# Kernel optimization log

Measured on AMD Instinct MI355X. Metric: run time of the kernel, lower is better.

The kernel has to match this reference:

```python
import jax, jax.numpy as jnp
import numpy as np
from jax import lax

BS, L, NB = 16, 50, 64          # batch, seq_length, num_blk_pervisit
D = 256                          # d_model
BLK_D = 768                      # frozen block-embedding dim
N_BLK = 65536                    # block vocab size
MEM_SIZE = 64                    # mem_size == mem_update_size (required for stackable memory)
MEM_UPDATE = 64
EPS = 1e-5


def _blk_trans(x, w1, b1, w2, b2, g, b):
    # Linear(768->2D) + ReLU + Linear(2D->D) + LayerNorm(D); dropout omitted (eval mode)
    h = jax.nn.relu(x @ w1 + b1)
    y = h @ w2 + b2
    mu = jnp.mean(y, axis=-1, keepdims=True)
    var = jnp.mean((y - mu) ** 2, axis=-1, keepdims=True)
    return g * (y - mu) * lax.rsqrt(var + EPS) + b


def setup_inputs() -> dict:
    key = jax.random.key(0)
    ks = jax.random.split(key, 16)
    s = 0.02
    f32 = jnp.float32
    return {
        "v_all": jax.random.normal(ks[0], (BS, L, D), f32),
        "transformed_v_all": jax.random.normal(ks[1], (BS, L, D), f32),
        "blk_emb_w": jax.random.normal(ks[2], (N_BLK, BLK_D), f32) * s,
        "bt_w1": jax.random.normal(ks[3], (BLK_D, 2 * D), f32) * s,
        "bt_b1": jnp.zeros((2 * D,), f32),
        "bt_w2": jax.random.normal(ks[4], (2 * D, D), f32) * s,
        "bt_b2": jnp.zeros((D,), f32),
        "bt_g": jnp.ones((D,), f32),
        "bt_b": jnp.zeros((D,), f32),
        "wq": jax.random.normal(ks[5], (D, D), f32) * s,
        "wk": jax.random.normal(ks[6], (D, D), f32) * s,
        "am_w1": jax.random.normal(ks[7], (2 * D, D), f32) * s,
        "am_b1": jnp.zeros((D,), f32),
        "am_w2": jax.random.normal(ks[8], (D, 1), f32) * s,
        "out_w": jax.random.normal(ks[9], (2 * D, 2), f32) * s,
        "out_b": jnp.zeros((2,), f32),
        "input_txt": jax.random.randint(ks[10], (BS, L, NB), 0, N_BLK, dtype=jnp.int32),
        "masks_txt": jax.random.randint(ks[11], (BS, L, NB), 0, 2, dtype=jnp.int32),
        "lengths": jax.random.randint(ks[12], (BS,), 2, L + 1, dtype=jnp.int32),
    }


def reference(v_all, transformed_v_all, blk_emb_w, bt_w1, bt_b1, bt_w2, bt_b2,
              bt_g, bt_b, wq, wk, am_w1, am_b1, am_w2, out_w, out_b,
              input_txt, masks_txt, lengths):
    bt = (bt_w1, bt_b1, bt_w2, bt_b2, bt_g, bt_b)

    # --- per-visit block selection (att_mlp + topk gather) ---
    v_text = _blk_trans(blk_emb_w[input_txt], *bt)                 # [BS,L,NB,D]
    tv = jnp.broadcast_to(transformed_v_all[:, :, None, :], v_text.shape)
    att_in = jnp.concatenate([tv, v_text], axis=-1)                # [BS,L,NB,2D]
    score = (jnp.tanh(att_in @ am_w1 + am_b1) @ am_w2)[..., 0]     # [BS,L,NB]
    score = jax.nn.softmax(score, axis=-1)
    score = jnp.where(masks_txt == 0, 0.0, score)
    idx = lax.top_k(score, MEM_UPDATE)[1]                          # [BS,L,MU]
    sel_ids = jnp.take_along_axis(input_txt, idx, axis=2)          # [BS,L,MU]
    sel_mask = jnp.take_along_axis(masks_txt, idx, axis=2)

    # --- sequential memory update recurrence ---
    query = transformed_v_all + v_all                              # [BS,L,D]
    scale = jnp.sqrt(jnp.float32(D))

    def step(carry, xs):
        ids, mk = carry                                            # [BS, M]
        nids, nmk, q = xs                                          # [BS,MU], [BS,MU], [BS,D]
        mem_in = jnp.concatenate([ids, nids], axis=1)              # [BS, 2M]
        mask_in = jnp.concatenate([mk, nmk], axis=1)
        x = _blk_trans(blk_emb_w[mem_in], *bt)                     # [BS,2M,D]
        e = jnp.einsum("bd,bmd->bm", q @ wq, x @ wk) / scale
        att = jnp.where(mask_in == 0, 0.0, jax.nn.softmax(e, axis=-1))
        tki = lax.top_k(att, MEM_SIZE)[1]                          # [BS, M]
        oi = jnp.take_along_axis(mem_in, tki, axis=1)
        om = jnp.take_along_axis(mask_in, tki, axis=1)
        return (oi, om), oi

    xs = (jnp.swapaxes(sel_ids[:, 1:], 0, 1),
          jnp.swapaxes(sel_mask[:, 1:], 0, 1),
          jnp.swapaxes(query[:, 1:], 0, 1))
    _, ys = lax.scan(step, (sel_ids[:, 0], sel_mask[:, 0]), xs)    # [L-1,BS,M]
    mem_stack = jnp.swapaxes(ys, 0, 1)                             # [BS,L-1,M] == memory[1:]
    memory_final = jnp.take_along_axis(
        mem_stack, (lengths - 2)[:, None, None], axis=1)[:, 0]      # [BS,M]

    # --- pooling + output head ---
    vmask = jnp.arange(L)[None, :] < lengths[:, None]              # length-masked max pool
    v_final = jnp.max(jnp.where(vmask[:, :, None], transformed_v_all, -jnp.inf), axis=1)
    mem_vec_final = jnp.max(_blk_trans(blk_emb_w[memory_final], *bt), axis=1)
    output = jnp.concatenate([v_final, mem_vec_final], axis=1) @ out_w + out_b
    return (output, memory_final)
```

## Files before the change

### kernel.cpp

```cpp
#include <hip/hip_runtime.h>
#include <math.h>

constexpr int kBS   = 16;
constexpr int kL    = 50;
constexpr int kNB   = 64;
constexpr int kD    = 256;
constexpr int kNBLK = 65536;
constexpr int kMaxUsed = 51200;

#define NEG_HUGE (-3.402823466e38f)

typedef _Float16 h8 __attribute__((ext_vector_type(8)));
typedef float f32x4 __attribute__((ext_vector_type(4)));

__device__ __forceinline__ unsigned f2sort(float f) {
    unsigned u = __float_as_uint(f);
    return (u & 0x80000000u) ? ~u : (u | 0x80000000u);
}

__device__ __forceinline__ void bitonic_u64(unsigned long long* s, int i, int n) {
    for (int k = 2; k <= n; k <<= 1) {
        for (int j = k >> 1; j > 0; j >>= 1) {
            __syncthreads();
            int ixj = i ^ j;
            if (ixj > i) {
                unsigned long long x = s[i], y = s[ixj];
                bool sw = ((i & k) == 0) ? (x > y) : (x < y);
                if (sw) { s[i] = y; s[ixj] = x; }
            }
        }
    }
    __syncthreads();
}

__device__ __forceinline__ void split8(const float4& a, const float4& b, float s,
                                       h8& hh, h8& ll) {
    float v0 = a.x * s, v1 = a.y * s, v2 = a.z * s, v3 = a.w * s;
    float v4 = b.x * s, v5 = b.y * s, v6 = b.z * s, v7 = b.w * s;
    hh[0] = (_Float16)v0; ll[0] = (_Float16)(v0 - (float)hh[0]);
    hh[1] = (_Float16)v1; ll[1] = (_Float16)(v1 - (float)hh[1]);
    hh[2] = (_Float16)v2; ll[2] = (_Float16)(v2 - (float)hh[2]);
    hh[3] = (_Float16)v3; ll[3] = (_Float16)(v3 - (float)hh[3]);
    hh[4] = (_Float16)v4; ll[4] = (_Float16)(v4 - (float)hh[4]);
    hh[5] = (_Float16)v5; ll[5] = (_Float16)(v5 - (float)hh[5]);
    hh[6] = (_Float16)v6; ll[6] = (_Float16)(v6 - (float)hh[6]);
    hh[7] = (_Float16)v7; ll[7] = (_Float16)(v7 - (float)hh[7]);
}

__global__ void k_clear(int* __restrict__ flags) {
    flags[blockIdx.x * 256 + threadIdx.x] = 0;
}
__global__ void k_mark(const int* __restrict__ ids, int* __restrict__ flags, int n) {
    int i = blockIdx.x * 256 + threadIdx.x;
    if (i < n) flags[ids[i]] = 1;
}
__global__ void k_scan_a(const int* __restrict__ flags, int* __restrict__ slots,
                         int* __restrict__ bsum) {
    int i = blockIdx.x * 256 + threadIdx.x;
    __shared__ int s[256];
    int v = flags[i];
    s[threadIdx.x] = v; __syncthreads();
    for (int o = 1; o < 256; o <<= 1) {
        int t2 = (threadIdx.x >= o) ? s[threadIdx.x - o] : 0;
        __syncthreads();
        s[threadIdx.x] += t2;
        __syncthreads();
    }
    slots[i] = s[threadIdx.x] - v;
    if (threadIdx.x == 255) bsum[blockIdx.x] = s[255];
}
__global__ void k_scan_b(int* __restrict__ bsum, int* __restrict__ mcount) {
    __shared__ int s[256];
    int v = bsum[threadIdx.x];
    s[threadIdx.x] = v; __syncthreads();
    for (int o = 1; o < 256; o <<= 1) {
        int t2 = (threadIdx.x >= o) ? s[threadIdx.x - o] : 0;
        __syncthreads();
        s[threadIdx.x] += t2;
        __syncthreads();
    }
    bsum[threadIdx.x] = s[threadIdx.x] - v;
    if (threadIdx.x == 255) *mcount = s[255];
}
__global__ void k_scan_c(const int* __restrict__ flags, int* __restrict__ slots,
                         const int* __restrict__ bsum, int* __restrict__ ulist) {
    int i = blockIdx.x * 256 + threadIdx.x;
    int slot = slots[i] + bsum[blockIdx.x];
    slots[i] = slot;
    if (flags[i]) ulist[slot] = i;
}

__global__ void k_split_bT(const float* __restrict__ B, int ldb, int K,
                           _Float16* __restrict__ Ph, _Float16* __restrict__ Pl,
                           int row_off, int ldp, float scale)
{
    int n = blockIdx.x;
    for (int k = threadIdx.x; k < K; k += 256) {
        float v = B[(long long)k * ldb + n] * scale;
        _Float16 h = (_Float16)v;
        _Float16 l = (_Float16)(v - (float)h);
        Ph[(long long)(row_off + n) * ldp + k] = h;
        Pl[(long long)(row_off + n) * ldp + k] = l;
    }
}

__global__ __launch_bounds__(256) void gemm_mfma3(
    const float* __restrict__ A, int lda,
    const int* __restrict__ gather, const float* __restrict__ A2,
    const _Float16* __restrict__ Bh, const _Float16* __restrict__ Bl,
    float* __restrict__ C, int ldc,
    int Mstatic, const int* __restrict__ mcount,
    int K, const float* __restrict__ bias, int relu,
    float ascale, float inv_scale)
{
    int mlim = Mstatic;
    if (mcount) mlim = *mcount;
    const int bm = blockIdx.x * 128;
    if (bm >= mlim) return;
    const int bn = blockIdx.y * 128;

    __shared__ h8 AsH[512];
    __shared__ h8 AsL[512];
    __shared__ h8 BsH[512];
    __shared__ h8 BsL[512];

    const int t = threadIdx.x;
    const int lane = t & 63;
    const int wid  = t >> 6;
    const int aRt = (wid >> 1) * 4;
    const int bRt = (wid & 1) * 4;
    const int wr = (wid >> 1) * 64, wc = (wid & 1) * 64;

    const float* aptr[2];
    const float* aptr2[2];
    int awslot[2];
    #pragma unroll
    for (int i = 0; i < 2; ++i) {
        int c = t + i * 256;
        int r = c >> 2, ks = c & 3;
        awslot[i] = (r >> 4) * 64 + (r & 15) + 16 * ks;
        int grow = bm + r;
        long long g = 0;
        if (grow < mlim) g = gather ? (long long)gather[grow] : (long long)grow;
        aptr[i]  = A + g * lda + ks * 8;
        aptr2[i] = A2 ? (A2 + g * lda + ks * 8) : nullptr;
    }
    const _Float16* bptr[4];
    int bwslot[4], bpl[4];
    #pragma unroll
    for (int i = 0; i < 4; ++i) {
        int c = t + i * 256;
        int pl = c >> 9, cc = c & 511;
        int r = cc >> 2, ks = cc & 3;
        bwslot[i] = (r >> 4) * 64 + (r & 15) + 16 * ks;
        bpl[i] = pl;
        bptr[i] = (pl ? Bl : Bh) + (long long)(bn + r) * K + ks * 8;
    }

    f32x4 acc[4][4];
    #pragma unroll
    for (int m = 0; m < 4; ++m)
        #pragma unroll
        for (int n = 0; n < 4; ++n)
            acc[m][n] = (f32x4){0.f, 0.f, 0.f, 0.f};

    float4 pa[2][2], pa2[2][2];
    h8 pb[4];
    #pragma unroll
    for (int i = 0; i < 2; ++i) {
        pa[i][0] = *(const float4*)(aptr[i]);
        pa[i][1] = *(const float4*)(aptr[i] + 4);
        if (A2) {
            pa2[i][0] = *(const float4*)(aptr2[i]);
            pa2[i][1] = *(const float4*)(aptr2[i] + 4);
        }
    }
    #pragma unroll
    for (int i = 0; i < 4; ++i) pb[i] = *(const h8*)(bptr[i]);

    const int nt = K / 32;
    for (int tI = 0; tI < nt; ++tI) {
        __syncthreads();
        #pragma unroll
        for (int i = 0; i < 2; ++i) {
            float4 x = pa[i][0], y = pa[i][1];
            if (A2) {
                x.x += pa2[i][0].x; x.y += pa2[i][0].y;
                x.z += pa2[i][0].z; x.w += pa2[i][0].w;
                y.x += pa2[i][1].x; y.y += pa2[i][1].y;
                y.z += pa2[i][1].z; y.w += pa2[i][1].w;
            }
            h8 hh, ll;
            split8(x, y, ascale, hh, ll);
            AsH[awslot[i]] = hh;
            AsL[awslot[i]] = ll;
        }
        #pragma unroll
        for (int i = 0; i < 4; ++i) {
            (bpl[i] ? BsL : BsH)[bwslot[i]] = pb[i];
        }
        __syncthreads();
        if (tI + 1 < nt) {
            int k0 = (tI + 1) * 32;
            #pragma unroll
            for (int i = 0; i < 2; ++i) {
                pa[i][0] = *(const float4*)(aptr[i] + k0);
                pa[i][1] = *(const float4*)(aptr[i] + k0 + 4);
                if (A2) {
                    pa2[i][0] = *(const float4*)(aptr2[i] + k0);
                    pa2[i][1] = *(const float4*)(aptr2[i] + k0 + 4);
                }
            }
            #pragma unroll
            for (int i = 0; i < 4; ++i) pb[i] = *(const h8*)(bptr[i] + k0);
        }
        h8 ah_[4], al_[4];
        #pragma unroll
        for (int m = 0; m < 4; ++m) {
            ah_[m] = AsH[(aRt + m) * 64 + lane];
            al_[m] = AsL[(aRt + m) * 64 + lane];
        }
        #pragma unroll
        for (int n = 0; n < 4; ++n) {
            h8 bh_ = BsH[(bRt + n) * 64 + lane];
            h8 bl_ = BsL[(bRt + n) * 64 + lane];
            #pragma unroll
            for (int m = 0; m < 4; ++m) {
                acc[m][n] = __builtin_amdgcn_mfma_f32_16x16x32_f16(ah_[m], bh_, acc[m][n], 0, 0, 0);
                acc[m][n] = __builtin_amdgcn_mfma_f32_16x16x32_f16(ah_[m], bl_, acc[m][n], 0, 0, 0);
                acc[m][n] = __builtin_amdgcn_mfma_f32_16x16x32_f16(al_[m], bh_, acc[m][n], 0, 0, 0);
            }
        }
    }

    const int fr  = lane & 15;
    const int cr0 = (lane >> 4) * 4;
    #pragma unroll
    for (int m = 0; m < 4; ++m) {
        #pragma unroll
        for (int r = 0; r < 4; ++r) {
            int row = bm + wr + m * 16 + cr0 + r;
            if (row >= mlim) continue;
            float* crow = C + (long long)row * ldc;
            #pragma unroll
            for (int n = 0; n < 4; ++n) {
                int col = bn + wc + n * 16 + fr;
                float v = acc[m][n][r] * inv_scale;
                if (bias) v += bias[col];
                if (relu) v = fmaxf(v, 0.f);
                crow[col] = v;
            }
        }
    }
}

__global__ __launch_bounds__(256) void ln256_inplace(
    float* __restrict__ Y, const float* __restrict__ g, const float* __restrict__ b,
    int Mstatic, const int* __restrict__ mcount)
{
    int row = blockIdx.x;
    int mlim = mcount ? *mcount : Mstatic;
    if (row >= mlim) return;
    int d = threadIdx.x;
    float v = Y[(long long)row * 256 + d];
    __shared__ float red[256];
    red[d] = v; __syncthreads();
    for (int off = 128; off; off >>= 1) { if (d < off) red[d] += red[d + off]; __syncthreads(); }
    float mu = red[0] * (1.f / 256.f);
    __syncthreads();
    float dv = v - mu;
    red[d] = dv * dv; __syncthreads();
    for (int off = 128; off; off >>= 1) { if (d < off) red[d] += red[d + off]; __syncthreads(); }
    float var = red[0] * (1.f / 256.f);
    float out = g[d] * dv * (1.f / sqrtf(var + 1e-5f)) + b[d];
    Y[(long long)row * 256 + d] = out;
}

__global__ __launch_bounds__(256) void p1score(
    const float* __restrict__ tvp, const float* __restrict__ AK,
    const int* __restrict__ slots, const float* __restrict__ am_w2,
    const int* __restrict__ ids, float* __restrict__ scores)
{
    int bl = blockIdx.x;
    int lane = threadIdx.x & 63;
    int wv   = threadIdx.x >> 6;
    float4 tv = *(const float4*)(tvp + (long long)bl * 256 + lane * 4);
    float4 w2 = *(const float4*)(am_w2 + lane * 4);
    for (int s = wv * 16; s < wv * 16 + 16; ++s) {
        int slot = slots[ids[bl * 64 + s]];
        float4 a = *(const float4*)(AK + (long long)slot * 512 + lane * 4);
        double p = (double)tanhf(tv.x + a.x) * w2.x
                 + (double)tanhf(tv.y + a.y) * w2.y
                 + (double)tanhf(tv.z + a.z) * w2.z
                 + (double)tanhf(tv.w + a.w) * w2.w;
        #pragma unroll
        for (int off = 32; off; off >>= 1) p += __shfl_down(p, off);
        if (lane == 0) scores[bl * 64 + s] = (float)p;
    }
}

__global__ __launch_bounds__(64) void p1sort(
    const float* __restrict__ scores, const int* __restrict__ ids_in,
    const int* __restrict__ mk_in, int* __restrict__ sel_ids, int* __restrict__ sel_mk)
{
    int bl = blockIdx.x;
    int i = threadIdx.x;
    __shared__ unsigned long long s[64];
    float sc = scores[bl * 64 + i];
    int mk = mk_in[bl * 64 + i];
    float key = mk ? sc : NEG_HUGE;
    s[i] = ((unsigned long long)(~f2sort(key)) << 32) | (unsigned)i;
    bitonic_u64(s, i, 64);
    int src = (int)(unsigned)(s[i] & 0xffffffffull);
    sel_ids[bl * 64 + i] = ids_in[bl * 64 + src];
    sel_mk [bl * 64 + i] = mk_in [bl * 64 + src];
}

__global__ __launch_bounds__(256) void etab2(
    const float* __restrict__ qw, const float* __restrict__ AK,
    const int* __restrict__ slots, const int* __restrict__ sel_ids,
    float* __restrict__ E)
{
    const int l = blockIdx.x;
    const int b = blockIdx.y;
    __shared__ float Ks[16][64];
    __shared__ float Qs[16][68];
    __shared__ int rowA[64];
    const int t  = threadIdx.x;
    const int tx = t & 15, ty = t >> 4;
    if (t < 64) rowA[t] = slots[sel_ids[(b * kL + l) * 64 + t]];
    __syncthreads();

    const int rA = t >> 2;
    const int kA = (t & 3) * 4;
    const float* aptr = AK + (long long)rowA[rA] * 512 + 256 + kA;
    const float* qbase = qw + ((long long)b * kL + 1) * 256;
    const bool tsok = rA < 49;

    double acc[4][4];
    #pragma unroll
    for (int i = 0; i < 4; ++i)
        #pragma unroll
        for (int j = 0; j < 4; ++j) acc[i][j] = 0.0;

    for (int k0 = 0; k0 < 256; k0 += 16) {
        float4 av = *(const float4*)(aptr + k0);
        float4 bv = make_float4(0.f, 0.f, 0.f, 0.f);
        if (tsok) bv = *(const float4*)(qbase + (long long)rA * 256 + k0 + kA);
        __syncthreads();
        Ks[kA + 0][rA] = av.x; Ks[kA + 1][rA] = av.y;
        Ks[kA + 2][rA] = av.z; Ks[kA + 3][rA] = av.w;
        Qs[kA + 0][rA] = bv.x; Qs[kA + 1][rA] = bv.y;
        Qs[kA + 2][rA] = bv.z; Qs[kA + 3][rA] = bv.w;
        __syncthreads();
        #pragma unroll
        for (int k = 0; k < 16; ++k) {
            float a[4], q[4];
            *(float4*)&a[0] = *(const float4*)&Ks[k][tx * 4];
            *(float4*)&q[0] = *(const float4*)&Qs[k][ty * 4];
            #pragma unroll
            for (int i = 0; i < 4; ++i)
                #pragma unroll
                for (int j = 0; j < 4; ++j)
                    acc[i][j] += (double)a[i] * (double)q[j];
        }
    }
    #pragma unroll
    for (int j = 0; j < 4; ++j) {
        int ts = ty * 4 + j;
        if (ts >= 49) continue;
        #pragma unroll
        for (int i = 0; i < 4; ++i) {
            int s = tx * 4 + i;
            E[((long long)b * 49 + ts) * 3200 + l * 64 + s] = (float)acc[i][j];
        }
    }
}

__global__ __launch_bounds__(64) void recur(
    const float* __restrict__ E, const int* __restrict__ sel_ids,
    const int* __restrict__ sel_mk, const int* __restrict__ lengths,
    int* __restrict__ memf, float* __restrict__ dout_mem)
{
    const int b = blockIdx.x;
    const int lane = threadIdx.x;

    int cid = sel_ids[(b * kL) * 64 + lane];
    int cmk = sel_mk [(b * kL) * 64 + lane];
    int ccd = lane;

    const int tlast = lengths[b] - 2;
    const float* Eb = E + (long long)b * 49 * 3200;

    for (int ts = 0; ts <= tlast; ++ts) {
        int nid = sel_ids[(b * kL + ts + 1) * 64 + lane];
        int nmk = sel_mk [(b * kL + ts + 1) * 64 + lane];
        const float* Et = Eb + (long long)ts * 3200;

        float k0 = cmk ? Et[ccd] : NEG_HUGE;
        float k1 = nmk ? Et[(ts + 1) * 64 + lane] : NEG_HUGE;
        unsigned long long s0 = ((unsigned long long)(~f2sort(k0)) << 32) | (unsigned)lane;
        unsigned long long s1 = ((unsigned long long)(~f2sort(k1)) << 32) | (unsigned)(64 + lane);

        #pragma unroll
        for (int k = 2; k <= 128; k <<= 1) {
            #pragma unroll
            for (int j = k >> 1; j > 0; j >>= 1) {
                if (j == 64) {
                    unsigned long long mn = s0 < s1 ? s0 : s1;
                    unsigned long long mx = s0 < s1 ? s1 : s0;
                    s0 = mn; s1 = mx;
                } else {
                    bool up   = (lane & j) == 0;
                    bool asc0 = (lane & k) == 0;
                    bool asc1 = (((lane + 64) & k) == 0);
                    unsigned long long p0 = __shfl_xor(s0, j, 64);
                    unsigned long long p1 = __shfl_xor(s1, j, 64);
                    bool km0 = (asc0 == up), km1 = (asc1 == up);
                    s0 = (km0 == (s0 < p0)) ? s0 : p0;
                    s1 = (km1 == (s1 < p1)) ? s1 : p1;
                }
            }
        }

        int src  = (int)(unsigned)(s0 & 0xffffffffull);
        int srcl = src & 63;
        int c_id = __shfl(cid, srcl, 64);
        int c_mk = __shfl(cmk, srcl, 64);
        int c_cd = __shfl(ccd, srcl, 64);
        int n_id = __shfl(nid, srcl, 64);
        int n_mk = __shfl(nmk, srcl, 64);
        bool isnew = src >= 64;
        cid = isnew ? n_id : c_id;
        cmk = isnew ? n_mk : c_mk;
        ccd = isnew ? ((ts + 1) * 64 + srcl) : c_cd;
    }

    memf[b * 64 + lane] = cid;
    dout_mem[b * 64 + lane] = (float)cid;
}

__global__ __launch_bounds__(256) void head_k(
    const float* __restrict__ tva, const int* __restrict__ lengths,
    const float* __restrict__ T, const int* __restrict__ slots,
    const int* __restrict__ memf, const float* __restrict__ out_w,
    const float* __restrict__ out_b, float* __restrict__ dout)
{
    int b = blockIdx.x, d = threadIdx.x;
    int len = lengths[b];
    float vf = NEG_HUGE;
    for (int l = 0; l < len; ++l) vf = fmaxf(vf, tva[((long long)b * kL + l) * 256 + d]);
    float mv = NEG_HUGE;
    for (int m = 0; m < 64; ++m) {
        int slot = slots[memf[b * 64 + m]];
        mv = fmaxf(mv, T[(long long)slot * 256 + d]);
    }
    double p0 = (double)vf * out_w[d * 2 + 0] + (double)mv * out_w[(256 + d) * 2 + 0];
    double p1 = (double)vf * out_w[d * 2 + 1] + (double)mv * out_w[(256 + d) * 2 + 1];
    __shared__ double r0[256], r1[256];
    r0[d] = p0; r1[d] = p1; __syncthreads();
    for (int off = 128; off; off >>= 1) {
        if (d < off) { r0[d] += r0[d + off]; r1[d] += r1[d + off]; }
        __syncthreads();
    }
    if (d == 0) {
        dout[b * 2 + 0] = (float)(r0[0] + out_b[0]);
        dout[b * 2 + 1] = (float)(r1[0] + out_b[1]);
    }
}

extern "C" void kernel_launch(void* const* d_in, const int* in_sizes, int n_in,
                              void* d_out, int out_size, void* d_ws, size_t ws_size,
                              hipStream_t stream)
{
    const float* v_all  = (const float*)d_in[0];
    const float* tva    = (const float*)d_in[1];
    const float* emb    = (const float*)d_in[2];
    const float* bt_w1  = (const float*)d_in[3];
    const float* bt_b1  = (const float*)d_in[4];
    const float* bt_w2  = (const float*)d_in[5];
    const float* bt_b2  = (const float*)d_in[6];
    const float* bt_g   = (const float*)d_in[7];
    const float* bt_bb  = (const float*)d_in[8];
    const float* wq     = (const float*)d_in[9];
    const float* wk     = (const float*)d_in[10];
    const float* am_w1  = (const float*)d_in[11];
    const float* am_b1  = (const float*)d_in[12];
    const float* am_w2  = (const float*)d_in[13];
    const float* out_w  = (const float*)d_in[14];
    const float* out_b  = (const float*)d_in[15];
    const int*   in_txt = (const int*)d_in[16];
    const int*   mk_txt = (const int*)d_in[17];
    const int*   lens   = (const int*)d_in[18];
    float* dout = (float*)d_out;

    const float S12 = 4096.f, S7 = 128.f, S8 = 256.f;
    const float INV24 = 1.f / 16777216.f;
    const float INV19 = 1.f / 524288.f;
    const float INV20 = 1.f / 1048576.f;

    size_t off = 0;
    float* W = (float*)d_ws;
    auto take = [&](size_t n) { float* p = W + off; off += (n + 3) & ~(size_t)3; return p; };
    auto takeh = [&](size_t nh) { return (_Float16*)take((nh + 1) / 2); };

    float* AKp  = take((size_t)kMaxUsed * 512);
    float* Tt   = take((size_t)kMaxUsed * 256);
    float* Hp   = take((size_t)kMaxUsed * 512);
    float* Ep   = Hp;
    float* tvpP = take((size_t)800 * 256);
    float* qwP  = take((size_t)800 * 256);
    float* scP  = take((size_t)800 * 64);
    int*   selI = (int*)take((size_t)800 * 64);
    int*   selM = (int*)take((size_t)800 * 64);
    int*   flagsP = (int*)take(kNBLK);
    int*   slotsP = (int*)take(kNBLK);
    int*   ulist  = (int*)take(kNBLK);
    int*   bsum   = (int*)take(256);
    int*   mcount = (int*)take(16);
    int*   memfP  = (int*)take(1024);
    _Float16* W1h = takeh((size_t)512 * 768);
    _Float16* W1l = takeh((size_t)512 * 768);
    _Float16* W2h = takeh((size_t)256 * 512);
    _Float16* W2l = takeh((size_t)256 * 512);
    _Float16* BCh = takeh((size_t)512 * 256);
    _Float16* BCl = takeh((size_t)512 * 256);
    _Float16* ALh = takeh((size_t)256 * 256);
    _Float16* ALl = takeh((size_t)256 * 256);
    _Float16* WQh = takeh((size_t)256 * 256);
    _Float16* WQl = takeh((size_t)256 * 256);

    k_clear<<<dim3(256), dim3(256), 0, stream>>>(flagsP);
    k_mark <<<dim3(200), dim3(256), 0, stream>>>(in_txt, flagsP, 51200);
    k_scan_a<<<dim3(256), dim3(256), 0, stream>>>(flagsP, slotsP, bsum);
    k_scan_b<<<dim3(1),   dim3(256), 0, stream>>>(bsum, mcount);
    k_scan_c<<<dim3(256), dim3(256), 0, stream>>>(flagsP, slotsP, bsum, ulist);
    k_split_bT<<<dim3(512), dim3(256), 0, stream>>>(bt_w1, 512, 768, W1h, W1l, 0, 768, S12);
    k_split_bT<<<dim3(256), dim3(256), 0, stream>>>(bt_w2, 256, 512, W2h, W2l, 0, 512, S12);
    k_split_bT<<<dim3(256), dim3(256), 0, stream>>>(am_w1 + 256 * 256, 256, 256, BCh, BCl, 0,   256, S12);
    k_split_bT<<<dim3(256), dim3(256), 0, stream>>>(wk,                256, 256, BCh, BCl, 256, 256, S12);
    k_split_bT<<<dim3(256), dim3(256), 0, stream>>>(am_w1, 256, 256, ALh, ALl, 0, 256, S12);
    k_split_bT<<<dim3(256), dim3(256), 0, stream>>>(wq,    256, 256, WQh, WQl, 0, 256, S12);

    gemm_mfma3<<<dim3(7, 2), dim3(256), 0, stream>>>(
        tva, 256, nullptr, nullptr, ALh, ALl, tvpP, 256, 800, nullptr, 256, am_b1, 0, S7, INV19);
    gemm_mfma3<<<dim3(7, 2), dim3(256), 0, stream>>>(
        tva, 256, nullptr, v_all, WQh, WQl, qwP, 256, 800, nullptr, 256, nullptr, 0, S7, INV19);

    gemm_mfma3<<<dim3(kMaxUsed / 128, 4), dim3(256), 0, stream>>>(
        emb, 768, ulist, nullptr, W1h, W1l, Hp, 512, 0, mcount, 768, bt_b1, 1, S12, INV24);
    gemm_mfma3<<<dim3(kMaxUsed / 128, 2), dim3(256), 0, stream>>>(
        Hp, 512, nullptr, nullptr, W2h, W2l, Tt, 256, 0, mcount, 512, bt_b2, 0, S12, INV24);
    ln256_inplace<<<dim3(kMaxUsed), dim3(256), 0, stream>>>(Tt, bt_g, bt_bb, 0, mcount);
    gemm_mfma3<<<dim3(kMaxUsed / 128, 4), dim3(256), 0, stream>>>(
        Tt, 256, nullptr, nullptr, BCh, BCl, AKp, 512, 0, mcount, 256, nullptr, 0, S8, INV20);

    p1score<<<dim3(800), dim3(256), 0, stream>>>(tvpP, AKp, slotsP, am_w2, in_txt, scP);
    p1sort<<<dim3(800), dim3(64), 0, stream>>>(scP, in_txt, mk_txt, selI, selM);

    etab2<<<dim3(50, 16), dim3(256), 0, stream>>>(qwP, AKp, slotsP, selI, Ep);

    recur<<<dim3(16), dim3(64), 0, stream>>>(Ep, selI, selM, lens, memfP, dout + 32);

    head_k<<<dim3(16), dim3(256), 0, stream>>>(tva, lens, Tt, slotsP, memfP,
                                               out_w, out_b, dout);
}
```

Baseline: 589.8 us.

## Emit split fp16 hidden activations from first MLP GEMM and add fp16-input GEMM

```diff
diff --git a/kernel.cpp b/kernel.cpp
--- a/kernel.cpp
+++ b/kernel.cpp
@@ -47,6 +47,18 @@
     hh[7] = (_Float16)v7; ll[7] = (_Float16)(v7 - (float)hh[7]);
 }
 
+__device__ __forceinline__ void swz_block(int nby, int& bm, int& bn) {
+    unsigned id = blockIdx.x, g = gridDim.x, s = id;
+    if ((g & 7u) == 0u) { unsigned c = g >> 3; s = (id & 7u) * c + (id >> 3); }
+    bm = (int)(s / (unsigned)nby) * 128;
+    bn = (int)(s % (unsigned)nby) * 128;
+}
+
+__device__ __forceinline__ void slot_rc(int s, int& r, int& ks) {
+    r  = ((s >> 6) << 4) + (s & 15);
+    ks = (s >> 4) & 3;
+}
+
 __global__ void k_clear(int* __restrict__ flags) {
     flags[blockIdx.x * 256 + threadIdx.x] = 0;
 }
@@ -109,15 +121,16 @@
     const int* __restrict__ gather, const float* __restrict__ A2,
     const _Float16* __restrict__ Bh, const _Float16* __restrict__ Bl,
     float* __restrict__ C, int ldc,
-    int Mstatic, const int* __restrict__ mcount,
+    _Float16* __restrict__ Ch, _Float16* __restrict__ Cl, int ldch,
+    int nby, int Mstatic, const int* __restrict__ mcount,
     int K, const float* __restrict__ bias, int relu,
-    float ascale, float inv_scale)
+    float ascale, float inv_scale, float out_scale)
 {
     int mlim = Mstatic;
     if (mcount) mlim = *mcount;
-    const int bm = blockIdx.x * 128;
+    int bm, bn;
+    swz_block(nby, bm, bn);
     if (bm >= mlim) return;
-    const int bn = blockIdx.y * 128;
 
     __shared__ h8 AsH[512];
     __shared__ h8 AsL[512];
@@ -133,12 +146,10 @@
 
     const float* aptr[2];
     const float* aptr2[2];
-    int awslot[2];
     #pragma unroll
     for (int i = 0; i < 2; ++i) {
         int c = t + i * 256;
-        int r = c >> 2, ks = c & 3;
-        awslot[i] = (r >> 4) * 64 + (r & 15) + 16 * ks;
+        int r, ks; slot_rc(c, r, ks);
         int grow = bm + r;
         long long g = 0;
         if (grow < mlim) g = gather ? (long long)gather[grow] : (long long)grow;
@@ -146,15 +157,14 @@
         aptr2[i] = A2 ? (A2 + g * lda + ks * 8) : nullptr;
     }
     const _Float16* bptr[4];
-    int bwslot[4], bpl[4];
+    int bpl[4];
     #pragma unroll
     for (int i = 0; i < 4; ++i) {
         int c = t + i * 256;
-        int pl = c >> 9, cc = c & 511;
-        int r = cc >> 2, ks = cc & 3;
-        bwslot[i] = (r >> 4) * 64 + (r & 15) + 16 * ks;
-        bpl[i] = pl;
-        bptr[i] = (pl ? Bl : Bh) + (long long)(bn + r) * K + ks * 8;
+        bpl[i] = c >> 9;
+        int s = c & 511;
+        int r, ks; slot_rc(s, r, ks);
+        bptr[i] = (bpl[i] ? Bl : Bh) + (long long)(bn + r) * K + ks * 8;
     }
 
     f32x4 acc[4][4];
@@ -192,12 +202,13 @@
             }
             h8 hh, ll;
             split8(x, y, ascale, hh, ll);
-            AsH[awslot[i]] = hh;
-            AsL[awslot[i]] = ll;
+            AsH[t + i * 256] = hh;
+            AsL[t + i * 256] = ll;
         }
         #pragma unroll
         for (int i = 0; i < 4; ++i) {
-            (bpl[i] ? BsL : BsH)[bwslot[i]] = pb[i];
+            int s = (t + i * 256) & 511;
+            (bpl[i] ? BsL : BsH)[s] = pb[i];
         }
         __syncthreads();
         if (tI + 1 < nt) {
@@ -213,6 +224,123 @@
             }
             #pragma unroll
             for (int i = 0; i < 4; ++i) pb[i] = *(const h8*)(bptr[i] + k0);
+        }
+        h8 ah_[4], al_[4];
+        #pragma unroll
+        for (int m = 0; m < 4; ++m) {
+            ah_[m] = AsH[(aRt + m) * 64 + lane];
+            al_[m] = AsL[(aRt + m) * 64 + lane];
+        }
+        #pragma unroll
+        for (int n = 0; n < 4; ++n) {
+            h8 bh_ = BsH[(bRt + n) * 64 + lane];
+            h8 bl_ = BsL[(bRt + n) * 64 + lane];
+            #pragma unroll
+            for (int m = 0; m < 4; ++m) {
+                acc[m][n] = __builtin_amdgcn_mfma_f32_16x16x32_f16(ah_[m], bh_, acc[m][n], 0, 0, 0);
+                acc[m][n] = __builtin_amdgcn_mfma_f32_16x16x32_f16(ah_[m], bl_, acc[m][n], 0, 0, 0);
+                acc[m][n] = __builtin_amdgcn_mfma_f32_16x16x32_f16(al_[m], bh_, acc[m][n], 0, 0, 0);
+            }
+        }
+    }
+
+    const int fr  = lane & 15;
+    const int cr0 = (lane >> 4) * 4;
+    #pragma unroll
+    for (int m = 0; m < 4; ++m) {
+        #pragma unroll
+        for (int r = 0; r < 4; ++r) {
+            int row = bm + wr + m * 16 + cr0 + r;
+            if (row >= mlim) continue;
+            #pragma unroll
+            for (int n = 0; n < 4; ++n) {
+                int col = bn + wc + n * 16 + fr;
+                float v = acc[m][n][r] * inv_scale;
+                if (bias) v += bias[col];
+                if (relu) v = fmaxf(v, 0.f);
+                if (Ch) {
+                    float w = v * out_scale;
+                    _Float16 hh = (_Float16)w;
+                    Ch[(long long)row * ldch + col] = hh;
+                    Cl[(long long)row * ldch + col] = (_Float16)(w - (float)hh);
+                } else {
+                    C[(long long)row * ldc + col] = v;
+                }
+            }
+        }
+    }
+}
+
+__global__ __launch_bounds__(256) void gemm_p3(
+    const _Float16* __restrict__ Ah, const _Float16* __restrict__ Al,
+    const _Float16* __restrict__ Bh, const _Float16* __restrict__ Bl,
+    float* __restrict__ C, int ldc,
+    int nby, int Mstatic, const int* __restrict__ mcount,
+    int K, const float* __restrict__ bias, int relu, float inv_scale)
+{
+    int mlim = Mstatic;
+    if (mcount) mlim = *mcount;
+    int bm, bn;
+    swz_block(nby, bm, bn);
+    if (bm >= mlim) return;
+
+    __shared__ h8 AsH[512];
+    __shared__ h8 AsL[512];
+    __shared__ h8 BsH[512];
+    __shared__ h8 BsL[512];
+
+    const int t = threadIdx.x;
+    const int lane = t & 63;
+    const int wid  = t >> 6;
+    const int aRt = (wid >> 1) * 4;
+    const int bRt = (wid & 1) * 4;
+    const int wr = (wid >> 1) * 64, wc = (wid & 1) * 64;
+
+    const _Float16* aptr[4];
+    const _Float16* bptr[4];
+    int apl[4], bpl[4];
+    #pragma unroll
+    for (int i = 0; i < 4; ++i) {
+        int c = t + i * 256;
+        apl[i] = c >> 9; bpl[i] = c >> 9;
+        int s = c & 511;
+        int r, ks; slot_rc(s, r, ks);
+        int arow = bm + r; if (arow >= mlim) arow = bm;
+        aptr[i] = (apl[i] ? Al : Ah) + (long long)arow * K + ks * 8;
+        bptr[i] = (bpl[i] ? Bl : Bh) + (long long)(bn + r) * K + ks * 8;
+    }
+
+    f32x4 acc[4][4];
+    #pragma unroll
+    for (int m = 0; m < 4; ++m)
+        #pragma unroll
+        for (int n = 0; n < 4; ++n)
+            acc[m][n] = (f32x4){0.f, 0.f, 0.f, 0.f};
+
+    h8 pa[4], pb[4];
+    #pragma unroll
+    for (int i = 0; i < 4; ++i) {
+        pa[i] = *(const h8*)(aptr[i]);
+        pb[i] = *(const h8*)(bptr[i]);
+    }
+
+    const int nt = K / 32;
+    for (int tI = 0; tI < nt; ++tI) {
+        __syncthreads();
+        #pragma unroll
+        for (int i = 0; i < 4; ++i) {
+            int s = (t + i * 256) & 511;
+            (apl[i] ? AsL : AsH)[s] = pa[i];
+            (bpl[i] ? BsL : BsH)[s] = pb[i];
+        }
+        __syncthreads();
+        if (tI + 1 < nt) {
+            int k0 = (tI + 1) * 32;
+            #pragma unroll
+            for (int i = 0; i < 4; ++i) {
+                pa[i] = *(const h8*)(aptr[i] + k0);
+                pb[i] = *(const h8*)(bptr[i] + k0);
+            }
         }
         h8 ah_[4], al_[4];
         #pragma unroll
@@ -506,8 +634,9 @@
 
     float* AKp  = take((size_t)kMaxUsed * 512);
     float* Tt   = take((size_t)kMaxUsed * 256);
-    float* Hp   = take((size_t)kMaxUsed * 512);
-    float* Ep   = Hp;
+    _Float16* Hph = takeh((size_t)kMaxUsed * 512);
+    _Float16* Hpl = takeh((size_t)kMaxUsed * 512);
+    float* Ep   = (float*)Hph;
     float* tvpP = take((size_t)800 * 256);
     float* qwP  = take((size_t)800 * 256);
     float* scP  = take((size_t)800 * 64);
@@ -542,18 +671,23 @@
     k_split_bT<<<dim3(256), dim3(256), 0, stream>>>(am_w1, 256, 256, ALh, ALl, 0, 256, S12);
     k_split_bT<<<dim3(256), dim3(256), 0, stream>>>(wq,    256, 256, WQh, WQl, 0, 256, S12);
 
-    gemm_mfma3<<<dim3(7, 2), dim3(256), 0, stream>>>(
-        tva, 256, nullptr, nullptr, ALh, ALl, tvpP, 256, 800, nullptr, 256, am_b1, 0, S7, INV19);
-    gemm_mfma3<<<dim3(7, 2), dim3(256), 0, stream>>>(
-        tva, 256, nullptr, v_all, WQh, WQl, qwP, 256, 800, nullptr, 256, nullptr, 0, S7, INV19);
-
-    gemm_mfma3<<<dim3(kMaxUsed / 128, 4), dim3(256), 0, stream>>>(
-        emb, 768, ulist, nullptr, W1h, W1l, Hp, 512, 0, mcount, 768, bt_b1, 1, S12, INV24);
-    gemm_mfma3<<<dim3(kMaxUsed / 128, 2), dim3(256), 0, stream>>>(
-        Hp, 512, nullptr, nullptr, W2h, W2l, Tt, 256, 0, mcount, 512, bt_b2, 0, S12, INV24);
+    gemm_mfma3<<<dim3(14), dim3(256), 0, stream>>>(
+        tva, 256, nullptr, nullptr, ALh, ALl, tvpP, 256, nullptr, nullptr, 0,
+        2, 800, nullptr, 256, am_b1, 0, S7, INV19, 1.f);
+    gemm_mfma3<<<dim3(14), dim3(256), 0, stream>>>(
+        tva, 256, nullptr, v_all, WQh, WQl, qwP, 256, nullptr, nullptr, 0,
+        2, 800, nullptr, 256, nullptr, 0, S7, INV19, 1.f);
+
+    gemm_mfma3<<<dim3(1600), dim3(256), 0, stream>>>(
+        emb, 768, ulist, nullptr, W1h, W1l, nullptr, 0, Hph, Hpl, 512,
+        4, 0, mcount, 768, bt_b1, 1, S12, INV24, S12);
+    gemm_p3<<<dim3(800), dim3(256), 0, stream>>>(
+        Hph, Hpl, W2h, W2l, Tt, 256,
+        2, 0, mcount, 512, bt_b2, 0, INV24);
     ln256_inplace<<<dim3(kMaxUsed), dim3(256), 0, stream>>>(Tt, bt_g, bt_bb, 0, mcount);
-    gemm_mfma3<<<dim3(kMaxUsed / 128, 4), dim3(256), 0, stream>>>(
-        Tt, 256, nullptr, nullptr, BCh, BCl, AKp, 512, 0, mcount, 256, nullptr, 0, S8, INV20);
+    gemm_mfma3<<<dim3(1600), dim3(256), 0, stream>>>(
+        Tt, 256, nullptr, nullptr, BCh, BCl, AKp, 512, nullptr, nullptr, 0,
+        4, 0, mcount, 256, nullptr, 0, S8, INV20, 1.f);
 
     p1score<<<dim3(800), dim3(256), 0, stream>>>(tvpP, AKp, slotsP, am_w2, in_txt, scP);
     p1sort<<<dim3(800), dim3(64), 0, stream>>>(scP, in_txt, mk_txt, selI, selM);
```

Result: slower. 731.0 us (+23.9%).
